# Kernel optimization log

Measured on AMD Instinct MI355X. Metric: run time of the kernel, lower is better.

## Reference

```python
import jax, jax.numpy as jnp
import numpy as np
from jax import lax

B, S, D, H = 128, 256, 64, 512
H2 = 2 * H          # decoder / bi-encoder hidden size
GE = 4 * H          # encoder LSTM gate size (per direction)
GD = 4 * H2         # decoder LSTM gate size
T = 60              # hard-coded decode length


def _w(k, shape):
    return jax.random.normal(k, shape, dtype=jnp.float32) * 0.05


def setup_inputs() -> dict:
    ks = iter(jax.random.split(jax.random.key(0), 32))
    inp = {"x": jax.random.normal(next(ks), (B, S, D), jnp.float32)}
    inp["enc0_Wih"] = _w(next(ks), (2, GE, D))
    inp["enc0_Whh"] = _w(next(ks), (2, GE, H))
    inp["enc0_b"] = _w(next(ks), (2, GE))
    inp["enc1_Wih"] = _w(next(ks), (2, GE, H2))
    inp["enc1_Whh"] = _w(next(ks), (2, GE, H))
    inp["enc1_b"] = _w(next(ks), (2, GE))
    for n in ("attn1", "attn2", "attn3"):
        inp[n + "_W"] = _w(next(ks), (H2, H2))
        inp[n + "_b"] = _w(next(ks), (H2,))
    inp["dec1_Wih"] = _w(next(ks), (GD, H2 + D))
    inp["dec1_Whh"] = _w(next(ks), (GD, H2))
    inp["dec1_b"] = _w(next(ks), (GD,))
    inp["dec2_Wih"] = _w(next(ks), (GD, 2 * H2))
    inp["dec2_Whh"] = _w(next(ks), (GD, H2))
    inp["dec2_b"] = _w(next(ks), (GD,))
    inp["dec3_Wih"] = _w(next(ks), (GD, 2 * H2))
    inp["dec3_Whh"] = _w(next(ks), (GD, H2))
    inp["dec3_b"] = _w(next(ks), (GD,))
    inp["out_W"] = _w(next(ks), (D, H2))
    inp["out_b"] = _w(next(ks), (D,))
    return inp


def _lstm_gates(g, c):
    i, f, gg, o = jnp.split(g, 4, axis=-1)  # torch gate order: i, f, g, o
    c = jax.nn.sigmoid(f) * c + jax.nn.sigmoid(i) * jnp.tanh(gg)
    h = jax.nn.sigmoid(o) * jnp.tanh(c)
    return h, c


def _lstm_layer(x, Wih, Whh, b, reverse):
    # x: [B,S,Din] -> hidden sequence [B,S,Hn]
    Bn = x.shape[0]
    Hn = Whh.shape[1]
    xg = jnp.einsum('bsd,gd->bsg', x, Wih) + b  # precompute input contributions

    def step(carry, xt):
        h, c = carry
        h, c = _lstm_gates(xt + h @ Whh.T, c)
        return (h, c), h

    init = (jnp.zeros((Bn, Hn), x.dtype), jnp.zeros((Bn, Hn), x.dtype))
    _, hs = lax.scan(step, init, jnp.swapaxes(xg, 0, 1), reverse=reverse)
    return jnp.swapaxes(hs, 0, 1)


def _bilstm(x, Wih, Whh, b):
    fwd = _lstm_layer(x, Wih[0], Whh[0], b[0], False)
    bwd = _lstm_layer(x, Wih[1], Whh[1], b[1], True)
    return jnp.concatenate([fwd, bwd], axis=-1)


def _cell(inp, h, c, Wih, Whh, b):
    return _lstm_gates(inp @ Wih.T + h @ Whh.T + b, c)


def _forward(x, enc0_Wih, enc0_Whh, enc0_b, enc1_Wih, enc1_Whh, enc1_b,
             attn1_W, attn1_b, attn2_W, attn2_b, attn3_W, attn3_b,
             dec1_Wih, dec1_Whh, dec1_b, dec2_Wih, dec2_Whh, dec2_b,
             dec3_Wih, dec3_Whh, dec3_b, out_W, out_b):
    Bn = x.shape[0]
    enc_out = _bilstm(_bilstm(x, enc0_Wih, enc0_Whh, enc0_b),
                      enc1_Wih, enc1_Whh, enc1_b)          # [B,S,2H]
    keys1 = enc_out @ attn1_W.T + attn1_b                  # [B,S,2H]
    keys2 = enc_out @ attn2_W.T + attn2_b
    keys3 = enc_out @ attn3_W.T + attn3_b

    def attend(h, keys):
        a = jax.nn.softmax(jnp.einsum('bd,bsd->bs', h, keys), axis=-1)
        return jnp.einsum('bs,bsd->bd', a, enc_out)        # [B,2H]

    z = jnp.zeros((Bn, H2), x.dtype)
    carry0 = (z, z, z, z, z, z, x[:, -1, :])

    def step(carry, _):
        h1, c1, h2, c2, h3, c3, prev = carry
        ctx1 = attend(h1, keys1)
        h1, c1 = _cell(jnp.concatenate([ctx1, prev], -1), h1, c1,
                       dec1_Wih, dec1_Whh, dec1_b)
        ctx2 = attend(h2, keys2)
        h2, c2 = _cell(jnp.concatenate([ctx2, h1], -1), h2, c2,
                       dec2_Wih, dec2_Whh, dec2_b)
        ctx3 = attend(h3, keys3)
        h3, c3 = _cell(jnp.concatenate([ctx3, h2], -1), h3, c3,
                       dec3_Wih, dec3_Whh, dec3_b)
        yt = h3 @ out_W.T + out_b                          # [B,D]
        return (h1, c1, h2, c2, h3, c3, yt), yt

    _, ys = lax.scan(step, carry0, None, length=T)         # [T,B,D]
    return jnp.swapaxes(ys, 0, 1)                          # [B,T,D]


def reference(x, enc0_Wih, enc0_Whh, enc0_b, enc1_Wih, enc1_Whh, enc1_b,
              attn1_W, attn1_b, attn2_W, attn2_b, attn3_W, attn3_b,
              dec1_Wih, dec1_Whh, dec1_b, dec2_Wih, dec2_Whh, dec2_b,
              dec3_Wih, dec3_Whh, dec3_b, out_W, out_b):
    return _forward(x, enc0_Wih, enc0_Whh, enc0_b, enc1_Wih, enc1_Whh, enc1_b,
                    attn1_W, attn1_b, attn2_W, attn2_b, attn3_W, attn3_b,
                    dec1_Wih, dec1_Whh, dec1_b, dec2_Wih, dec2_Whh, dec2_b,
                    dec3_Wih, dec3_Whh, dec3_b, out_W, out_b)
```

## Files before the change

### kernel.cpp

```cpp
#include <hip/hip_runtime.h>

typedef unsigned short u16;
typedef unsigned int u32;
typedef short v8s __attribute__((ext_vector_type(8)));
typedef float v4f __attribute__((ext_vector_type(4)));

#define DEV static __device__ __forceinline__

DEV float bf2f(u16 u) { union { u32 i; float f; } v; v.i = ((u32)u) << 16; return v.f; }
DEV u16 f2bf(float f) {
  union { float f; u32 i; } v; v.f = f;
  u32 i = v.i + 0x7FFFu + ((v.i >> 16) & 1u);
  return (u16)(i >> 16);
}
DEV float sigm(float x) { return 1.0f / (1.0f + __expf(-x)); }
DEV v4f mfma16(v8s a, v8s b, v4f c) {
  return __builtin_amdgcn_mfma_f32_16x16x32_bf16(a, b, c, 0, 0, 0);
}
DEV v8s ld8(const u16* p) { return *(const v8s*)p; }

DEV void gbar(u32* flags, int nwg, int wg, u32 tgt) {
  __syncthreads();
  if (threadIdx.x < 64) {
    if (threadIdx.x == 0) {
      __threadfence();
      __hip_atomic_store(flags + wg, tgt, __ATOMIC_RELEASE, __HIP_MEMORY_SCOPE_AGENT);
    }
    const int lane = threadIdx.x;
    for (;;) {
      bool ok = true;
      for (int i = lane; i < nwg; i += 64) {
        u32 v = __hip_atomic_load(flags + i, __ATOMIC_RELAXED, __HIP_MEMORY_SCOPE_AGENT);
        ok &= (v >= tgt);
      }
      if (__ballot((int)ok) == ~0ull) break;
      __builtin_amdgcn_s_sleep(1);
    }
    __threadfence();
  }
  __syncthreads();
}

__global__ void k_zero(uint4* p, int n) {
  int i = blockIdx.x * 256 + threadIdx.x;
  if (i < n) p[i] = make_uint4(0, 0, 0, 0);
}

__global__ void k_cvt(const float* __restrict__ s, u16* __restrict__ d, int n) {
  int i = (blockIdx.x * 256 + threadIdx.x) * 4;
  if (i < n) {
    float4 v = *(const float4*)(s + i);
    ushort4 u;
    u.x = f2bf(v.x); u.y = f2bf(v.y); u.z = f2bf(v.z); u.w = f2bf(v.w);
    *(ushort4*)(d + i) = u;
  }
}

__global__ void k_pack_enc(const float* __restrict__ Wih, const float* __restrict__ Whh,
                           const float* __restrict__ bsrc, u16* __restrict__ Wf,
                           float* __restrict__ bf, int DIN) {
  const int K = DIN + 512;
  const int bx = blockIdx.x;
  const int dir = bx >> 11, r = bx & 2047;
  const int g = (r >> 2) & 3, j = ((r >> 4) << 2) | (r & 3);
  const int orig = g * 512 + j;
  const float* wi = Wih + ((size_t)dir * 2048 + orig) * DIN;
  const float* wh = Whh + ((size_t)dir * 2048 + orig) * 512;
  u16* dst = Wf + ((size_t)dir * 2048 + r) * K;
  for (int k = threadIdx.x; k < K; k += 256)
    dst[k] = f2bf(k < DIN ? wi[k] : wh[k - DIN]);
  if (threadIdx.x == 0) bf[dir * 2048 + r] = bsrc[dir * 2048 + orig];
}

__global__ void k_pack_decf(const float* __restrict__ Wih, const float* __restrict__ Whh,
                            const float* __restrict__ bsrc, u16* __restrict__ Wf,
                            float* __restrict__ bf, int KIN) {
  const int K = KIN + 1024;
  const int r = blockIdx.x;
  const int g = (r >> 2) & 3, j = ((r >> 4) << 2) | (r & 3);
  const int orig = g * 1024 + j;
  const float* wi = Wih + (size_t)orig * KIN;
  const float* wh = Whh + (size_t)orig * 1024;
  const int wgi = r >> 4, l15 = r & 15;
  u16* dst = Wf + (size_t)wgi * (size_t)(K >> 5) * 512;
  for (int k = threadIdx.x; k < K; k += 256) {
    float v = k < KIN ? wi[k] : wh[k - KIN];
    dst[(size_t)(k >> 5) * 512 + (((k >> 3) & 3) * 16 + l15) * 8 + (k & 7)] = f2bf(v);
  }
  if (threadIdx.x == 0) bf[r] = bsrc[orig];
}

__global__ void k_pack_attnT(const float* __restrict__ w1, const float* __restrict__ w2,
                             const float* __restrict__ w3, u16* __restrict__ WQ) {
  const int a = blockIdx.x >> 10, tix = blockIdx.x & 1023;
  const int ti = tix >> 5, tj = tix & 31;
  const float* Wsrc = a == 0 ? w1 : (a == 1 ? w2 : w3);
  __shared__ float tl[32][33];
  const int r = threadIdx.x >> 3, c4 = (threadIdx.x & 7) * 4;
  const float* src = Wsrc + (size_t)(ti * 32 + r) * 1024 + tj * 32 + c4;
#pragma unroll
  for (int k = 0; k < 4; ++k) tl[r][c4 + k] = src[k];
  __syncthreads();
  const int cl = threadIdx.x >> 3, d4 = (threadIdx.x & 7) * 4;
  ushort4 u;
  u.x = f2bf(tl[d4 + 0][cl]); u.y = f2bf(tl[d4 + 1][cl]);
  u.z = f2bf(tl[d4 + 2][cl]); u.w = f2bf(tl[d4 + 3][cl]);
  *(ushort4*)(WQ + ((size_t)a << 20) + (size_t)(tj * 32 + cl) * 1024 + ti * 32 + d4) = u;
}

__global__ __launch_bounds__(512, 1) void k_rec(
    const u16* __restrict__ in, int DIN,
    const u16* __restrict__ Wf, const float* __restrict__ bias,
    u16* __restrict__ XG, u16* __restrict__ hst, u16* __restrict__ outp,
    u32* __restrict__ flags) {
  const int K = DIN + 512;
  const int DINk = DIN >> 5;
  const int wg = blockIdx.x;
  const int dir = wg >> 7, nt = wg & 127;
  const int r0 = nt * 16;
  const int tid = threadIdx.x, w = tid >> 6, lane = tid & 63;
  const int l15 = lane & 15, qd = lane >> 4;

  __shared__ u16 wlds[48 * 512];
  __shared__ float glds[128][17];

  {
    const u16* Wd = Wf + ((size_t)(dir * 2048 + r0)) * K;
    const int cnt = 16 * (K >> 3);
    for (int idx = tid; idx < cnt; idx += 512) {
      const int row = idx & 15, c8 = idx >> 4;
      uint4 v = *(const uint4*)(Wd + (size_t)row * K + c8 * 8);
      *(uint4*)(wlds + ((size_t)(c8 >> 2) * 512 + ((c8 & 3) * 16 + row) * 8)) = v;
    }
  }
  const int pm = tid >> 2, jl = tid & 3;
  float bw[4];
#pragma unroll
  for (int g = 0; g < 4; ++g) bw[g] = bias[dir * 2048 + r0 + g * 4 + jl];
  float cst = 0.f;
  __syncthreads();

  u32 bt = 1;
  if (DIN == 64) {
    for (int t = 0; t < 256; ++t) {
      const int tt = dir ? (255 - t) : t;
      const int pb = t & 1;
      const u16* xp = in + ((size_t)(w * 16 + l15) * 256 + tt) * 64 + qd * 8;
      const u16* hp = hst + ((size_t)((dir * 2 + pb) * 128 + w * 16 + l15)) * 512 + qd * 8;
      v4f a0 = mfma16(ld8(xp), ld8(wlds + lane * 8), (v4f){0.f, 0.f, 0.f, 0.f});
      v4f a1 = mfma16(ld8(xp + 32), ld8(wlds + 512 + lane * 8), (v4f){0.f, 0.f, 0.f, 0.f});
#pragma unroll 4
      for (int kkb = 0; kkb < 16; kkb += 2) {
        a0 = mfma16(ld8(hp + kkb * 32), ld8(wlds + (2 + kkb) * 512 + lane * 8), a0);
        a1 = mfma16(ld8(hp + kkb * 32 + 32), ld8(wlds + (3 + kkb) * 512 + lane * 8), a1);
      }
#pragma unroll
      for (int r = 0; r < 4; ++r)
        glds[w * 16 + qd * 4 + r][l15] = a0[r] + a1[r];
      __syncthreads();
      {
        float gi = glds[pm][0 * 4 + jl] + bw[0];
        float gf = glds[pm][1 * 4 + jl] + bw[1];
        float gg = glds[pm][2 * 4 + jl] + bw[2];
        float go = glds[pm][3 * 4 + jl] + bw[3];
        float cc = sigm(gf) * cst + sigm(gi) * tanhf(gg);
        cst = cc;
        u16 hb = f2bf(sigm(go) * tanhf(cc));
        hst[((size_t)((dir * 2 + (pb ^ 1)) * 128 + pm)) * 512 + nt * 4 + jl] = hb;
        outp[((size_t)pm * 256 + tt) * 1024 + dir * 512 + nt * 4 + jl] = hb;
      }
      gbar(flags + dir * 128, 128, nt, bt++);
    }
  } else {
    for (int ch = 0; ch < 32; ++ch) {
      for (int ttl = 0; ttl < 8; ++ttl) {
        const int tt = dir ? (255 - ch * 8 - ttl) : (ch * 8 + ttl);
        const u16* ap = in + ((size_t)(w * 16 + l15) * 256 + tt) * DIN + qd * 8;
        v4f a0 = (v4f){0.f, 0.f, 0.f, 0.f}, a1 = a0;
#pragma unroll 4
        for (int kkb = 0; kkb < 32; kkb += 2) {
          a0 = mfma16(ld8(ap + kkb * 32), ld8(wlds + kkb * 512 + lane * 8), a0);
          a1 = mfma16(ld8(ap + kkb * 32 + 32), ld8(wlds + (kkb + 1) * 512 + lane * 8), a1);
        }
        u16* xo = XG + (((size_t)(dir * 8 + ttl) * 128 + nt) * 128 + w * 16 + qd * 4) * 16 + l15;
#pragma unroll
        for (int r = 0; r < 4; ++r) xo[r * 16] = f2bf(a0[r] + a1[r]);
      }
      for (int ts = 0; ts < 8; ++ts) {
        const int t = ch * 8 + ts;
        const int tt = dir ? (255 - t) : t;
        const int pb = t & 1;
        const u16* hp = hst + ((size_t)((dir * 2 + pb) * 128 + w * 16 + l15)) * 512 + qd * 8;
        v4f a0 = (v4f){0.f, 0.f, 0.f, 0.f}, a1 = a0;
#pragma unroll 4
        for (int kkb = 0; kkb < 16; kkb += 2) {
          a0 = mfma16(ld8(hp + kkb * 32), ld8(wlds + (32 + kkb) * 512 + lane * 8), a0);
          a1 = mfma16(ld8(hp + kkb * 32 + 32), ld8(wlds + (33 + kkb) * 512 + lane * 8), a1);
        }
        const u16* xi = XG + (((size_t)(dir * 8 + ts) * 128 + nt) * 128 + w * 16 + qd * 4) * 16 + l15;
#pragma unroll
        for (int r = 0; r < 4; ++r)
          glds[w * 16 + qd * 4 + r][l15] = a0[r] + a1[r] + bf2f(xi[r * 16]);
        __syncthreads();
        {
          float gi = glds[pm][0 * 4 + jl] + bw[0];
          float gf = glds[pm][1 * 4 + jl] + bw[1];
          float gg = glds[pm][2 * 4 + jl] + bw[2];
          float go = glds[pm][3 * 4 + jl] + bw[3];
          float cc = sigm(gf) * cst + sigm(gi) * tanhf(gg);
          cst = cc;
          u16 hb = f2bf(sigm(go) * tanhf(cc));
          hst[((size_t)((dir * 2 + (pb ^ 1)) * 128 + pm)) * 512 + nt * 4 + jl] = hb;
          outp[((size_t)pm * 256 + tt) * 1024 + dir * 512 + nt * 4 + jl] = hb;
        }
        gbar(flags + dir * 128, 128, nt, bt++);
      }
    }
  }
}

struct DecArgs {
  const float *x, *outb;
  float* dout;
  const u16 *eo, *wq, *wout, *wd1, *wd2, *wd3;
  const float *bd1, *bd2, *bd3;
  u16 *qp, *hd, *ad1, *ad2, *ad3;
  u32* flags;
};

union DecSm {
  struct { float glds[128][17]; } c;
  struct {
    u16 e[32][1032];
    float sbuf[8][16][4];
    float wl[32][4];
    float alpha[4];
    float lfin[4];
  } a;
};

__global__ __launch_bounds__(512, 1) void k_dec(DecArgs A) {
  const int wg = blockIdx.x, tid = threadIdx.x;
  const int w = tid >> 6, lane = tid & 63, l15 = lane & 15, qd = lane >> 4;
  __shared__ DecSm sm;
  u32 bt = 1;

  const int cm_ = tid >> 2, cjl = tid & 3;
  const float* BDs[3] = {A.bd1, A.bd2, A.bd3};
  float cbias[3][4];
#pragma unroll
  for (int ci = 0; ci < 3; ++ci)
#pragma unroll
    for (int g = 0; g < 4; ++g)
      cbias[ci][g] = BDs[ci][wg * 16 + g * 4 + cjl];
  float cstate[3] = {0.f, 0.f, 0.f};

  for (int t = 0; t <= 60; ++t) {
    const int p = t & 1;
    if (wg < 192) {
      const int a = wg / 64, nc0 = (wg & 63) * 16;
      const u16* Ab = A.hd + (size_t)((a * 2 + p) * 128 + w * 16 + l15) * 1024 + qd * 8;
      const u16* Bw = A.wq + ((size_t)a << 20) + (size_t)(nc0 + l15) * 1024 + qd * 8;
      v4f a0 = (v4f){0.f, 0.f, 0.f, 0.f}, a1 = a0;
#pragma unroll 4
      for (int kk = 0; kk < 1024; kk += 64) {
        a0 = mfma16(ld8(Ab + kk), ld8(Bw + kk), a0);
        a1 = mfma16(ld8(Ab + kk + 32), ld8(Bw + kk + 32), a1);
      }
#pragma unroll
      for (int r = 0; r < 4; ++r)
        A.qp[(size_t)(w * 16 + qd * 4 + r) * 16384 + a * 1024 + nc0 + l15] =
            f2bf(a0[r] + a1[r]);
    } else if (wg < 196) {
      const int mt4 = wg - 192;
      if (t == 0) {
        int base = (mt4 * 512 + tid) * 4;
        int b = base >> 6, o = base & 63;
        const float* xs = A.x + (size_t)b * 16384 + 255 * 64 + o;
        u16* dst = A.ad1 + (size_t)b * 2112 + 1024 + o;
#pragma unroll
        for (int k2 = 0; k2 < 4; ++k2) dst[k2] = f2bf(xs[k2]);
      } else {
        const int mb = mt4 * 32 + (w >> 2) * 16, nb = (w & 3) * 16;
        const u16* Ab = A.hd + (size_t)((2 * 2 + p) * 128 + mb + l15) * 1024 + qd * 8;
        const u16* Bw = A.wout + (size_t)(nb + l15) * 1024 + qd * 8;
        v4f a0 = (v4f){0.f, 0.f, 0.f, 0.f}, a1 = a0;
#pragma unroll 4
        for (int kk = 0; kk < 1024; kk += 64) {
          a0 = mfma16(ld8(Ab + kk), ld8(Bw + kk), a0);
          a1 = mfma16(ld8(Ab + kk + 32), ld8(Bw + kk + 32), a1);
        }
        const int o = nb + l15;
        const float bo = A.outb[o];
#pragma unroll
        for (int r = 0; r < 4; ++r) {
          int m = mb + qd * 4 + r;
          float y = a0[r] + a1[r] + bo;
          A.dout[(size_t)m * 3840 + (t - 1) * 64 + o] = y;
          A.ad1[(size_t)m * 2112 + 1024 + o] = f2bf(y);
        }
      }
    }
    gbar(A.flags, 256, wg, bt++);
    if (t == 60) break;

    if (wg < 128) {
      const int b = wg;
      const u16* eob = A.eo + (size_t)b * 256 * 1024;
      v8s qf[8];
      {
        const u16* qsrc = A.qp + (size_t)b * 16384 + (size_t)l15 * 1024 + (w & 3) * 256 + qd * 8;
#pragma unroll
        for (int i = 0; i < 8; ++i) qf[i] = ld8(qsrc + i * 32);
      }
      const int d0 = w * 128 + lane * 2;
      float pv[3][2] = {{0.f, 0.f}, {0.f, 0.f}, {0.f, 0.f}};
      float mml0 = -3e38f, mml1 = -3e38f, mml2 = -3e38f;
      float lll0 = 0.f, lll1 = 0.f, lll2 = 0.f;
      const int sr = tid >> 4, sc = (tid & 15) * 8;
#pragma unroll
      for (int i = 0; i < 8; ++i)
        *(uint4*)&sm.a.e[sr][sc + i * 128] =
            *(const uint4*)(eob + (size_t)sr * 1024 + sc + i * 128);
      __syncthreads();

      for (int c = 0; c < 8; ++c) {
        uint4 pf[8];
        if (c < 7) {
          const u16* src = eob + (size_t)((c + 1) * 32 + sr) * 1024 + sc;
#pragma unroll
          for (int i = 0; i < 8; ++i) pf[i] = *(const uint4*)(src + i * 128);
        }
        {
          v4f sa = (v4f){0.f, 0.f, 0.f, 0.f};
          const u16* eb = &sm.a.e[(w >> 2) * 16 + l15][(w & 3) * 256 + qd * 8];
#pragma unroll
          for (int i = 0; i < 8; ++i) sa = mfma16(qf[i], ld8(eb + i * 32), sa);
          if (lane < 16) *(v4f*)&sm.a.sbuf[w][lane][0] = sa;
        }
        __syncthreads();
        if (tid < 32) {
          const int s = tid, sbb = s >> 4, sl = s & 15;
          float sc0 = 0.f, sc1 = 0.f, sc2 = 0.f;
#pragma unroll
          for (int k = 0; k < 4; ++k) {
            const float* sp = &sm.a.sbuf[sbb * 4 + k][sl][0];
            sc0 += sp[0]; sc1 += sp[1]; sc2 += sp[2];
          }
          float c0 = sc0, c1 = sc1, c2 = sc2;
#pragma unroll
          for (int m = 16; m >= 1; m >>= 1) {
            c0 = fmaxf(c0, __shfl_xor(c0, m));
            c1 = fmaxf(c1, __shfl_xor(c1, m));
            c2 = fmaxf(c2, __shfl_xor(c2, m));
          }
          float n0 = fmaxf(mml0, c0), n1 = fmaxf(mml1, c1), n2 = fmaxf(mml2, c2);
          float a0 = __expf(mml0 - n0), a1 = __expf(mml1 - n1), a2 = __expf(mml2 - n2);
          mml0 = n0; mml1 = n1; mml2 = n2;
          float w0 = __expf(sc0 - n0), w1 = __expf(sc1 - n1), w2 = __expf(sc2 - n2);
          sm.a.wl[s][0] = w0; sm.a.wl[s][1] = w1; sm.a.wl[s][2] = w2;
          float t0 = w0, t1 = w1, t2 = w2;
#pragma unroll
          for (int m = 16; m >= 1; m >>= 1) {
            t0 += __shfl_xor(t0, m); t1 += __shfl_xor(t1, m); t2 += __shfl_xor(t2, m);
          }
          lll0 = lll0 * a0 + t0; lll1 = lll1 * a1 + t1; lll2 = lll2 * a2 + t2;
          if (s == 0) {
            sm.a.alpha[0] = a0; sm.a.alpha[1] = a1; sm.a.alpha[2] = a2;
            sm.a.lfin[0] = lll0; sm.a.lfin[1] = lll1; sm.a.lfin[2] = lll2;
          }
        }
        __syncthreads();
        {
          const float a0 = sm.a.alpha[0], a1 = sm.a.alpha[1], a2 = sm.a.alpha[2];
          pv[0][0] *= a0; pv[0][1] *= a0;
          pv[1][0] *= a1; pv[1][1] *= a1;
          pv[2][0] *= a2; pv[2][1] *= a2;
#pragma unroll 4
          for (int s = 0; s < 32; ++s) {
            const float w0 = sm.a.wl[s][0], w1 = sm.a.wl[s][1], w2 = sm.a.wl[s][2];
            u32 ee = *(const u32*)&sm.a.e[s][d0];
            float e0 = bf2f((u16)ee), e1 = bf2f((u16)(ee >> 16));
            pv[0][0] += w0 * e0; pv[0][1] += w0 * e1;
            pv[1][0] += w1 * e0; pv[1][1] += w1 * e1;
            pv[2][0] += w2 * e0; pv[2][1] += w2 * e1;
          }
        }
        __syncthreads();
        if (c < 7) {
#pragma unroll
          for (int i = 0; i < 8; ++i)
            *(uint4*)&sm.a.e[sr][sc + i * 128] = pf[i];
        }
        __syncthreads();
      }
      {
        const float il0 = 1.0f / sm.a.lfin[0], il1 = 1.0f / sm.a.lfin[1],
                    il2 = 1.0f / sm.a.lfin[2];
        u32 p0 = (u32)f2bf(pv[0][0] * il0) | ((u32)f2bf(pv[0][1] * il0) << 16);
        u32 p1 = (u32)f2bf(pv[1][0] * il1) | ((u32)f2bf(pv[1][1] * il1) << 16);
        u32 p2 = (u32)f2bf(pv[2][0] * il2) | ((u32)f2bf(pv[2][1] * il2) << 16);
        *(u32*)&A.ad1[(size_t)b * 2112 + d0] = p0;
        *(u32*)&A.ad2[(size_t)b * 3072 + d0] = p1;
        *(u32*)&A.ad3[(size_t)b * 3072 + d0] = p2;
      }
    } else {
      const int b = wg - 128;
      const u16* h1 = A.hd + (size_t)((0 * 2 + p) * 128 + b) * 1024;
      const u16* h2 = A.hd + (size_t)((1 * 2 + p) * 128 + b) * 1024;
      const u16* h3 = A.hd + (size_t)((2 * 2 + p) * 128 + b) * 1024;
      if (tid < 128) {
        *(uint4*)(A.ad1 + (size_t)b * 2112 + 1088 + tid * 8) = *(const uint4*)(h1 + tid * 8);
      } else if (tid < 256) {
        int c8 = tid - 128;
        *(uint4*)(A.ad2 + (size_t)b * 3072 + 2048 + c8 * 8) = *(const uint4*)(h2 + c8 * 8);
      } else if (tid < 384) {
        int c8 = tid - 256;
        *(uint4*)(A.ad3 + (size_t)b * 3072 + 2048 + c8 * 8) = *(const uint4*)(h3 + c8 * 8);
      }
    }
    gbar(A.flags, 256, wg, bt++);

#pragma unroll
    for (int ci = 0; ci < 3; ++ci) {
      const int Kc = (ci == 0) ? 2112 : 3072;
      const u16* wb = (ci == 0 ? A.wd1 : ci == 1 ? A.wd2 : A.wd3) +
                      (size_t)wg * (size_t)(Kc >> 5) * 512;
      const u16* Ac = (ci == 0 ? A.ad1 : ci == 1 ? A.ad2 : A.ad3);
      {
        const u16* Ab = Ac + (size_t)(w * 16 + l15) * Kc + qd * 8;
        v4f a0 = (v4f){0.f, 0.f, 0.f, 0.f}, a1 = a0;
        const int NKB = Kc >> 5;
#pragma unroll 4
        for (int kkb = 0; kkb < NKB; kkb += 2) {
          a0 = mfma16(ld8(Ab + kkb * 32), ld8(wb + kkb * 512 + lane * 8), a0);
          a1 = mfma16(ld8(Ab + kkb * 32 + 32), ld8(wb + (kkb + 1) * 512 + lane * 8), a1);
        }
#pragma unroll
        for (int r = 0; r < 4; ++r)
          sm.c.glds[w * 16 + qd * 4 + r][l15] = a0[r] + a1[r];
      }
      __syncthreads();
      {
        float gi = sm.c.glds[cm_][0 * 4 + cjl] + cbias[ci][0];
        float gf = sm.c.glds[cm_][1 * 4 + cjl] + cbias[ci][1];
        float gg = sm.c.glds[cm_][2 * 4 + cjl] + cbias[ci][2];
        float go = sm.c.glds[cm_][3 * 4 + cjl] + cbias[ci][3];
        float cv = sigm(gf) * cstate[ci] + sigm(gi) * tanhf(gg);
        cstate[ci] = cv;
        u16 hb = f2bf(sigm(go) * tanhf(cv));
        const int jg = wg * 4 + cjl;
        A.hd[(size_t)((ci * 2 + (p ^ 1)) * 128 + cm_) * 1024 + jg] = hb;
        if (ci == 0) A.ad2[(size_t)cm_ * 3072 + 1024 + jg] = hb;
        else if (ci == 1) A.ad3[(size_t)cm_ * 3072 + 1024 + jg] = hb;
      }
      gbar(A.flags, 256, wg, bt++);
    }
  }
}

extern "C" void kernel_launch(void* const* d_in, const int* in_sizes, int n_in,
                              void* d_out, int out_size, void* d_ws, size_t ws_size,
                              hipStream_t stream) {
  char* ws = (char*)d_ws;
  size_t off = 0;
  auto alc = [&](size_t bytes) -> char* {
    char* pp = ws + off;
    off += (bytes + 255) & ~(size_t)255;
    return pp;
  };
  u16* XB = (u16*)alc(2097152ull * 2);
  u16* WF0 = (u16*)alc(2359296ull * 2);
  float* BF0 = (float*)alc(4096ull * 4);
  u16* WF1 = (u16*)alc(6291456ull * 2);
  float* BF1 = (float*)alc(4096ull * 4);
  u16* H0 = (u16*)alc(33554432ull * 2);
  u16* EO = (u16*)alc(33554432ull * 2);
  u16* HS0 = (u16*)alc(262144ull * 2);
  u16* HS1 = (u16*)alc(262144ull * 2);
  u16* XG = (u16*)alc(4194304ull * 2);
  u16* WQ = (u16*)alc(3145728ull * 2);
  u16* WOUT = (u16*)alc(65536ull * 2);
  u16* WD1 = (u16*)alc(8650752ull * 2);
  float* BD1 = (float*)alc(4096ull * 4);
  u16* WD2 = (u16*)alc(12582912ull * 2);
  float* BD2 = (float*)alc(4096ull * 4);
  u16* WD3 = (u16*)alc(12582912ull * 2);
  float* BD3 = (float*)alc(4096ull * 4);
  u16* QP = (u16*)alc(2097152ull * 2);
  u16* HD = (u16*)alc(786432ull * 2);
  u16* AD1 = (u16*)alc(270336ull * 2);
  u16* AD2 = (u16*)alc(393216ull * 2);
  u16* AD3 = (u16*)alc(393216ull * 2);
  u32* FLAGS = (u32*)alc(1536ull * 4);

  k_zero<<<2, 256, 0, stream>>>((uint4*)FLAGS, 384);
  k_zero<<<1024, 256, 0, stream>>>((uint4*)QP, 262144);
  k_zero<<<128, 256, 0, stream>>>((uint4*)HS0, 32768);
  k_zero<<<128, 256, 0, stream>>>((uint4*)HS1, 32768);
  k_zero<<<384, 256, 0, stream>>>((uint4*)HD, 98304);

  k_cvt<<<2048, 256, 0, stream>>>((const float*)d_in[0], XB, 2097152);
  k_cvt<<<64, 256, 0, stream>>>((const float*)d_in[22], WOUT, 65536);
  k_pack_enc<<<4096, 256, 0, stream>>>((const float*)d_in[1], (const float*)d_in[2],
                                       (const float*)d_in[3], WF0, BF0, 64);
  k_pack_enc<<<4096, 256, 0, stream>>>((const float*)d_in[4], (const float*)d_in[5],
                                       (const float*)d_in[6], WF1, BF1, 1024);
  k_pack_attnT<<<3072, 256, 0, stream>>>((const float*)d_in[7], (const float*)d_in[9],
                                         (const float*)d_in[11], WQ);
  k_pack_decf<<<4096, 256, 0, stream>>>((const float*)d_in[13], (const float*)d_in[14],
                                        (const float*)d_in[15], WD1, BD1, 1088);
  k_pack_decf<<<4096, 256, 0, stream>>>((const float*)d_in[16], (const float*)d_in[17],
                                        (const float*)d_in[18], WD2, BD2, 2048);
  k_pack_decf<<<4096, 256, 0, stream>>>((const float*)d_in[19], (const float*)d_in[20],
                                        (const float*)d_in[21], WD3, BD3, 2048);

  k_rec<<<256, 512, 0, stream>>>(XB, 64, WF0, BF0, XG, HS0, H0, FLAGS);
  k_rec<<<256, 512, 0, stream>>>(H0, 1024, WF1, BF1, XG, HS1, EO, FLAGS + 256);

  DecArgs da;
  da.x = (const float*)d_in[0];
  da.outb = (const float*)d_in[23];
  da.dout = (float*)d_out;
  da.eo = EO; da.wq = WQ; da.wout = WOUT;
  da.wd1 = WD1; da.wd2 = WD2; da.wd3 = WD3;
  da.bd1 = BD1; da.bd2 = BD2; da.bd3 = BD3;
  da.qp = QP; da.hd = HD; da.ad1 = AD1; da.ad2 = AD2; da.ad3 = AD3;
  da.flags = FLAGS + 512;
  k_dec<<<256, 512, 0, stream>>>(da);
}
```

Baseline: 29.97 ms.

## Replace grid-barrier fences with relaxed atomic data accesses and pack LSTM cell stores

Drops the __threadfence calls around the grid barrier and the release ordering on the flag store. In their place, all cross-workgroup data exchanged between barriers (hidden states, attention outputs, query projections, decoder inputs) is read and written through agent-scope relaxed atomic loads and stores. The LSTM cell update now has each thread compute two adjacent hidden units and write packed 32-bit values. Query and output-projection results are staged through LDS so they go out as wider stores. The aim is to cut per-step fence and barrier latency in the sequential recurrent loops, but memory-ordering correctness now depends on relaxed atomics without explicit fences.

```diff
diff --git a/kernel.cpp b/kernel.cpp
--- a/kernel.cpp
+++ b/kernel.cpp
@@ -2,6 +2,7 @@
 
 typedef unsigned short u16;
 typedef unsigned int u32;
+typedef unsigned long long u64;
 typedef short v8s __attribute__((ext_vector_type(8)));
 typedef float v4f __attribute__((ext_vector_type(4)));
 
@@ -19,13 +20,27 @@
 }
 DEV v8s ld8(const u16* p) { return *(const v8s*)p; }
 
+DEV u64 ldg64(const u16* p) {
+  return __hip_atomic_load((const u64*)p, __ATOMIC_RELAXED, __HIP_MEMORY_SCOPE_AGENT);
+}
+DEV void stg32(u16* p, u32 v) {
+  __hip_atomic_store((u32*)p, v, __ATOMIC_RELAXED, __HIP_MEMORY_SCOPE_AGENT);
+}
+DEV void stg64(u16* p, u64 v) {
+  __hip_atomic_store((u64*)p, v, __ATOMIC_RELAXED, __HIP_MEMORY_SCOPE_AGENT);
+}
+DEV v8s ld8c(const u16* p) {
+  union { u64 q[2]; v8s v; } u;
+  u.q[0] = ldg64(p);
+  u.q[1] = ldg64(p + 4);
+  return u.v;
+}
+
 DEV void gbar(u32* flags, int nwg, int wg, u32 tgt) {
   __syncthreads();
+  if (threadIdx.x == 0)
+    __hip_atomic_store(flags + wg, tgt, __ATOMIC_RELAXED, __HIP_MEMORY_SCOPE_AGENT);
   if (threadIdx.x < 64) {
-    if (threadIdx.x == 0) {
-      __threadfence();
-      __hip_atomic_store(flags + wg, tgt, __ATOMIC_RELEASE, __HIP_MEMORY_SCOPE_AGENT);
-    }
     const int lane = threadIdx.x;
     for (;;) {
       bool ok = true;
@@ -36,7 +51,6 @@
       if (__ballot((int)ok) == ~0ull) break;
       __builtin_amdgcn_s_sleep(1);
     }
-    __threadfence();
   }
   __syncthreads();
 }
@@ -114,7 +128,6 @@
     u16* __restrict__ XG, u16* __restrict__ hst, u16* __restrict__ outp,
     u32* __restrict__ flags) {
   const int K = DIN + 512;
-  const int DINk = DIN >> 5;
   const int wg = blockIdx.x;
   const int dir = wg >> 7, nt = wg & 127;
   const int r0 = nt * 16;
@@ -133,11 +146,14 @@
       *(uint4*)(wlds + ((size_t)(c8 >> 2) * 512 + ((c8 & 3) * 16 + row) * 8)) = v;
     }
   }
-  const int pm = tid >> 2, jl = tid & 3;
-  float bw[4];
-#pragma unroll
-  for (int g = 0; g < 4; ++g) bw[g] = bias[dir * 2048 + r0 + g * 4 + jl];
-  float cst = 0.f;
+  const int pm = tid >> 1, jp = tid & 1;
+  float bw[4][2];
+#pragma unroll
+  for (int g = 0; g < 4; ++g)
+#pragma unroll
+    for (int jj = 0; jj < 2; ++jj)
+      bw[g][jj] = bias[dir * 2048 + r0 + g * 4 + jp * 2 + jj];
+  float cst[2] = {0.f, 0.f};
   __syncthreads();
 
   u32 bt = 1;
@@ -151,23 +167,29 @@
       v4f a1 = mfma16(ld8(xp + 32), ld8(wlds + 512 + lane * 8), (v4f){0.f, 0.f, 0.f, 0.f});
 #pragma unroll 4
       for (int kkb = 0; kkb < 16; kkb += 2) {
-        a0 = mfma16(ld8(hp + kkb * 32), ld8(wlds + (2 + kkb) * 512 + lane * 8), a0);
-        a1 = mfma16(ld8(hp + kkb * 32 + 32), ld8(wlds + (3 + kkb) * 512 + lane * 8), a1);
+        a0 = mfma16(ld8c(hp + kkb * 32), ld8(wlds + (2 + kkb) * 512 + lane * 8), a0);
+        a1 = mfma16(ld8c(hp + kkb * 32 + 32), ld8(wlds + (3 + kkb) * 512 + lane * 8), a1);
       }
 #pragma unroll
       for (int r = 0; r < 4; ++r)
         glds[w * 16 + qd * 4 + r][l15] = a0[r] + a1[r];
       __syncthreads();
-      {
-        float gi = glds[pm][0 * 4 + jl] + bw[0];
-        float gf = glds[pm][1 * 4 + jl] + bw[1];
-        float gg = glds[pm][2 * 4 + jl] + bw[2];
-        float go = glds[pm][3 * 4 + jl] + bw[3];
-        float cc = sigm(gf) * cst + sigm(gi) * tanhf(gg);
-        cst = cc;
-        u16 hb = f2bf(sigm(go) * tanhf(cc));
-        hst[((size_t)((dir * 2 + (pb ^ 1)) * 128 + pm)) * 512 + nt * 4 + jl] = hb;
-        outp[((size_t)pm * 256 + tt) * 1024 + dir * 512 + nt * 4 + jl] = hb;
+      if (tid < 256) {
+        float hv2[2];
+#pragma unroll
+        for (int jj = 0; jj < 2; ++jj) {
+          const int jl = jp * 2 + jj;
+          float gi = glds[pm][0 * 4 + jl] + bw[0][jj];
+          float gf = glds[pm][1 * 4 + jl] + bw[1][jj];
+          float gg = glds[pm][2 * 4 + jl] + bw[2][jj];
+          float go = glds[pm][3 * 4 + jl] + bw[3][jj];
+          float cc = sigm(gf) * cst[jj] + sigm(gi) * tanhf(gg);
+          cst[jj] = cc;
+          hv2[jj] = sigm(go) * tanhf(cc);
+        }
+        u32 hv = (u32)f2bf(hv2[0]) | ((u32)f2bf(hv2[1]) << 16);
+        stg32(hst + ((size_t)((dir * 2 + (pb ^ 1)) * 128 + pm)) * 512 + nt * 4 + jp * 2, hv);
+        *(u32*)(outp + ((size_t)pm * 256 + tt) * 1024 + dir * 512 + nt * 4 + jp * 2) = hv;
       }
       gbar(flags + dir * 128, 128, nt, bt++);
     }
@@ -175,7 +197,7 @@
     for (int ch = 0; ch < 32; ++ch) {
       for (int ttl = 0; ttl < 8; ++ttl) {
         const int tt = dir ? (255 - ch * 8 - ttl) : (ch * 8 + ttl);
-        const u16* ap = in + ((size_t)(w * 16 + l15) * 256 + tt) * DIN + qd * 8;
+        const u16* ap = in + ((size_t)(w * 16 + l15) * 256 + tt) * 1024 + qd * 8;
         v4f a0 = (v4f){0.f, 0.f, 0.f, 0.f}, a1 = a0;
 #pragma unroll 4
         for (int kkb = 0; kkb < 32; kkb += 2) {
@@ -194,24 +216,30 @@
         v4f a0 = (v4f){0.f, 0.f, 0.f, 0.f}, a1 = a0;
 #pragma unroll 4
         for (int kkb = 0; kkb < 16; kkb += 2) {
-          a0 = mfma16(ld8(hp + kkb * 32), ld8(wlds + (32 + kkb) * 512 + lane * 8), a0);
-          a1 = mfma16(ld8(hp + kkb * 32 + 32), ld8(wlds + (33 + kkb) * 512 + lane * 8), a1);
+          a0 = mfma16(ld8c(hp + kkb * 32), ld8(wlds + (32 + kkb) * 512 + lane * 8), a0);
+          a1 = mfma16(ld8c(hp + kkb * 32 + 32), ld8(wlds + (33 + kkb) * 512 + lane * 8), a1);
         }
         const u16* xi = XG + (((size_t)(dir * 8 + ts) * 128 + nt) * 128 + w * 16 + qd * 4) * 16 + l15;
 #pragma unroll
         for (int r = 0; r < 4; ++r)
           glds[w * 16 + qd * 4 + r][l15] = a0[r] + a1[r] + bf2f(xi[r * 16]);
         __syncthreads();
-        {
-          float gi = glds[pm][0 * 4 + jl] + bw[0];
-          float gf = glds[pm][1 * 4 + jl] + bw[1];
-          float gg = glds[pm][2 * 4 + jl] + bw[2];
-          float go = glds[pm][3 * 4 + jl] + bw[3];
-          float cc = sigm(gf) * cst + sigm(gi) * tanhf(gg);
-          cst = cc;
-          u16 hb = f2bf(sigm(go) * tanhf(cc));
-          hst[((size_t)((dir * 2 + (pb ^ 1)) * 128 + pm)) * 512 + nt * 4 + jl] = hb;
-          outp[((size_t)pm * 256 + tt) * 1024 + dir * 512 + nt * 4 + jl] = hb;
+        if (tid < 256) {
+          float hv2[2];
+#pragma unroll
+          for (int jj = 0; jj < 2; ++jj) {
+            const int jl = jp * 2 + jj;
+            float gi = glds[pm][0 * 4 + jl] + bw[0][jj];
+            float gf = glds[pm][1 * 4 + jl] + bw[1][jj];
+            float gg = glds[pm][2 * 4 + jl] + bw[2][jj];
+            float go = glds[pm][3 * 4 + jl] + bw[3][jj];
+            float cc = sigm(gf) * cst[jj] + sigm(gi) * tanhf(gg);
+            cst[jj] = cc;
+            hv2[jj] = sigm(go) * tanhf(cc);
+          }
+          u32 hv = (u32)f2bf(hv2[0]) | ((u32)f2bf(hv2[1]) << 16);
+          stg32(hst + ((size_t)((dir * 2 + (pb ^ 1)) * 128 + pm)) * 512 + nt * 4 + jp * 2, hv);
+          *(u32*)(outp + ((size_t)pm * 256 + tt) * 1024 + dir * 512 + nt * 4 + jp * 2) = hv;
         }
         gbar(flags + dir * 128, 128, nt, bt++);
       }
@@ -230,6 +258,7 @@
 
 union DecSm {
   struct { float glds[128][17]; } c;
+  struct { float yb[32][65]; } y;
   struct {
     u16 e[32][1032];
     float sbuf[8][16][4];
@@ -245,15 +274,17 @@
   __shared__ DecSm sm;
   u32 bt = 1;
 
-  const int cm_ = tid >> 2, cjl = tid & 3;
+  const int cm_ = tid >> 1, cjp = tid & 1;
   const float* BDs[3] = {A.bd1, A.bd2, A.bd3};
-  float cbias[3][4];
+  float cbias[3][4][2];
 #pragma unroll
   for (int ci = 0; ci < 3; ++ci)
 #pragma unroll
     for (int g = 0; g < 4; ++g)
-      cbias[ci][g] = BDs[ci][wg * 16 + g * 4 + cjl];
-  float cstate[3] = {0.f, 0.f, 0.f};
+#pragma unroll
+      for (int jj = 0; jj < 2; ++jj)
+        cbias[ci][g][jj] = BDs[ci][wg * 16 + g * 4 + cjp * 2 + jj];
+  float cstate[3][2] = {{0.f, 0.f}, {0.f, 0.f}, {0.f, 0.f}};
 
   for (int t = 0; t <= 60; ++t) {
     const int p = t & 1;
@@ -264,13 +295,22 @@
       v4f a0 = (v4f){0.f, 0.f, 0.f, 0.f}, a1 = a0;
 #pragma unroll 4
       for (int kk = 0; kk < 1024; kk += 64) {
-        a0 = mfma16(ld8(Ab + kk), ld8(Bw + kk), a0);
-        a1 = mfma16(ld8(Ab + kk + 32), ld8(Bw + kk + 32), a1);
+        a0 = mfma16(ld8c(Ab + kk), ld8(Bw + kk), a0);
+        a1 = mfma16(ld8c(Ab + kk + 32), ld8(Bw + kk + 32), a1);
       }
 #pragma unroll
       for (int r = 0; r < 4; ++r)
-        A.qp[(size_t)(w * 16 + qd * 4 + r) * 16384 + a * 1024 + nc0 + l15] =
-            f2bf(a0[r] + a1[r]);
+        sm.c.glds[w * 16 + qd * 4 + r][l15] = a0[r] + a1[r];
+      __syncthreads();
+      {
+        const int m = tid >> 2, c4 = (tid & 3) * 4;
+        const float* row = &sm.c.glds[m][0];
+        u32 lo = (u32)f2bf(row[c4]) | ((u32)f2bf(row[c4 + 1]) << 16);
+        u32 hi = (u32)f2bf(row[c4 + 2]) | ((u32)f2bf(row[c4 + 3]) << 16);
+        u16* qdst = A.qp + (size_t)m * 16384 + a * 1024 + nc0 + c4;
+        stg32(qdst, lo);
+        stg32(qdst + 2, hi);
+      }
     } else if (wg < 196) {
       const int mt4 = wg - 192;
       if (t == 0) {
@@ -278,8 +318,8 @@
         int b = base >> 6, o = base & 63;
         const float* xs = A.x + (size_t)b * 16384 + 255 * 64 + o;
         u16* dst = A.ad1 + (size_t)b * 2112 + 1024 + o;
-#pragma unroll
-        for (int k2 = 0; k2 < 4; ++k2) dst[k2] = f2bf(xs[k2]);
+        stg32(dst, (u32)f2bf(xs[0]) | ((u32)f2bf(xs[1]) << 16));
+        stg32(dst + 2, (u32)f2bf(xs[2]) | ((u32)f2bf(xs[3]) << 16));
       } else {
         const int mb = mt4 * 32 + (w >> 2) * 16, nb = (w & 3) * 16;
         const u16* Ab = A.hd + (size_t)((2 * 2 + p) * 128 + mb + l15) * 1024 + qd * 8;
@@ -287,17 +327,24 @@
         v4f a0 = (v4f){0.f, 0.f, 0.f, 0.f}, a1 = a0;
 #pragma unroll 4
         for (int kk = 0; kk < 1024; kk += 64) {
-          a0 = mfma16(ld8(Ab + kk), ld8(Bw + kk), a0);
-          a1 = mfma16(ld8(Ab + kk + 32), ld8(Bw + kk + 32), a1);
-        }
-        const int o = nb + l15;
-        const float bo = A.outb[o];
-#pragma unroll
-        for (int r = 0; r < 4; ++r) {
-          int m = mb + qd * 4 + r;
-          float y = a0[r] + a1[r] + bo;
-          A.dout[(size_t)m * 3840 + (t - 1) * 64 + o] = y;
-          A.ad1[(size_t)m * 2112 + 1024 + o] = f2bf(y);
+          a0 = mfma16(ld8c(Ab + kk), ld8(Bw + kk), a0);
+          a1 = mfma16(ld8c(Ab + kk + 32), ld8(Bw + kk + 32), a1);
+        }
+        const int mloc = (w >> 2) * 16 + qd * 4;
+#pragma unroll
+        for (int r = 0; r < 4; ++r)
+          sm.y.yb[mloc + r][nb + l15] = a0[r] + a1[r] + A.outb[nb + l15];
+        __syncthreads();
+        {
+          const int ml = tid >> 4, c4 = (tid & 15) * 4;
+          const int mg = mt4 * 32 + ml;
+          float y0 = sm.y.yb[ml][c4], y1 = sm.y.yb[ml][c4 + 1];
+          float y2 = sm.y.yb[ml][c4 + 2], y3 = sm.y.yb[ml][c4 + 3];
+          float4 yv = {y0, y1, y2, y3};
+          *(float4*)(A.dout + (size_t)mg * 3840 + (t - 1) * 64 + c4) = yv;
+          u16* dst = A.ad1 + (size_t)mg * 2112 + 1024 + c4;
+          stg32(dst, (u32)f2bf(y0) | ((u32)f2bf(y1) << 16));
+          stg32(dst + 2, (u32)f2bf(y2) | ((u32)f2bf(y3) << 16));
         }
       }
     }
@@ -311,7 +358,7 @@
       {
         const u16* qsrc = A.qp + (size_t)b * 16384 + (size_t)l15 * 1024 + (w & 3) * 256 + qd * 8;
 #pragma unroll
-        for (int i = 0; i < 8; ++i) qf[i] = ld8(qsrc + i * 32);
+        for (int i = 0; i < 8; ++i) qf[i] = ld8c(qsrc + i * 32);
       }
       const int d0 = w * 128 + lane * 2;
       float pv[3][2] = {{0.f, 0.f}, {0.f, 0.f}, {0.f, 0.f}};
@@ -397,27 +444,26 @@
       {
         const float il0 = 1.0f / sm.a.lfin[0], il1 = 1.0f / sm.a.lfin[1],
                     il2 = 1.0f / sm.a.lfin[2];
-        u32 p0 = (u32)f2bf(pv[0][0] * il0) | ((u32)f2bf(pv[0][1] * il0) << 16);
-        u32 p1 = (u32)f2bf(pv[1][0] * il1) | ((u32)f2bf(pv[1][1] * il1) << 16);
-        u32 p2 = (u32)f2bf(pv[2][0] * il2) | ((u32)f2bf(pv[2][1] * il2) << 16);
-        *(u32*)&A.ad1[(size_t)b * 2112 + d0] = p0;
-        *(u32*)&A.ad2[(size_t)b * 3072 + d0] = p1;
-        *(u32*)&A.ad3[(size_t)b * 3072 + d0] = p2;
+        stg32(A.ad1 + (size_t)b * 2112 + d0,
+              (u32)f2bf(pv[0][0] * il0) | ((u32)f2bf(pv[0][1] * il0) << 16));
+        stg32(A.ad2 + (size_t)b * 3072 + d0,
+              (u32)f2bf(pv[1][0] * il1) | ((u32)f2bf(pv[1][1] * il1) << 16));
+        stg32(A.ad3 + (size_t)b * 3072 + d0,
+              (u32)f2bf(pv[2][0] * il2) | ((u32)f2bf(pv[2][1] * il2) << 16));
       }
     } else {
       const int b = wg - 128;
       const u16* h1 = A.hd + (size_t)((0 * 2 + p) * 128 + b) * 1024;
       const u16* h2 = A.hd + (size_t)((1 * 2 + p) * 128 + b) * 1024;
       const u16* h3 = A.hd + (size_t)((2 * 2 + p) * 128 + b) * 1024;
-      if (tid < 128) {
-        *(uint4*)(A.ad1 + (size_t)b * 2112 + 1088 + tid * 8) = *(const uint4*)(h1 + tid * 8);
-      } else if (tid < 256) {
-        int c8 = tid - 128;
-        *(uint4*)(A.ad2 + (size_t)b * 3072 + 2048 + c8 * 8) = *(const uint4*)(h2 + c8 * 8);
-      } else if (tid < 384) {
-        int c8 = tid - 256;
-        *(uint4*)(A.ad3 + (size_t)b * 3072 + 2048 + c8 * 8) = *(const uint4*)(h3 + c8 * 8);
-      }
+      if (tid < 256) {
+        stg64(A.ad1 + (size_t)b * 2112 + 1088 + tid * 4, ldg64(h1 + tid * 4));
+      } else if (tid < 512) {
+        int c4 = tid - 256;
+        stg64(A.ad2 + (size_t)b * 3072 + 2048 + c4 * 4, ldg64(h2 + c4 * 4));
+      }
+      if (tid < 256)
+        stg64(A.ad3 + (size_t)b * 3072 + 2048 + tid * 4, ldg64(h3 + tid * 4));
     }
     gbar(A.flags, 256, wg, bt++);
 
@@ -433,26 +479,32 @@
         const int NKB = Kc >> 5;
 #pragma unroll 4
         for (int kkb = 0; kkb < NKB; kkb += 2) {
-          a0 = mfma16(ld8(Ab + kkb * 32), ld8(wb + kkb * 512 + lane * 8), a0);
-          a1 = mfma16(ld8(Ab + kkb * 32 + 32), ld8(wb + (kkb + 1) * 512 + lane * 8), a1);
+          a0 = mfma16(ld8c(Ab + kkb * 32), ld8(wb + kkb * 512 + lane * 8), a0);
+          a1 = mfma16(ld8c(Ab + kkb * 32 + 32), ld8(wb + (kkb + 1) * 512 + lane * 8), a1);
         }
 #pragma unroll
         for (int r = 0; r < 4; ++r)
           sm.c.glds[w * 16 + qd * 4 + r][l15] = a0[r] + a1[r];
       }
       __syncthreads();
-      {
-        float gi = sm.c.glds[cm_][0 * 4 + cjl] + cbias[ci][0];
-        float gf = sm.c.glds[cm_][1 * 4 + cjl] + cbias[ci][1];
-        float gg = sm.c.glds[cm_][2 * 4 + cjl] + cbias[ci][2];
-        float go = sm.c.glds[cm_][3 * 4 + cjl] + cbias[ci][3];
-        float cv = sigm(gf) * cstate[ci] + sigm(gi) * tanhf(gg);
-        cstate[ci] = cv;
-        u16 hb = f2bf(sigm(go) * tanhf(cv));
-        const int jg = wg * 4 + cjl;
-        A.hd[(size_t)((ci * 2 + (p ^ 1)) * 128 + cm_) * 1024 + jg] = hb;
-        if (ci == 0) A.ad2[(size_t)cm_ * 3072 + 1024 + jg] = hb;
-        else if (ci == 1) A.ad3[(size_t)cm_ * 3072 + 1024 + jg] = hb;
+      if (tid < 256) {
+        float hv2[2];
+#pragma unroll
+        for (int jj = 0; jj < 2; ++jj) {
+          const int jl = cjp * 2 + jj;
+          float gi = sm.c.glds[cm_][0 * 4 + jl] + cbias[ci][0][jj];
+          float gf = sm.c.glds[cm_][1 * 4 + jl] + cbias[ci][1][jj];
+          float gg = sm.c.glds[cm_][2 * 4 + jl] + cbias[ci][2][jj];
+          float go = sm.c.glds[cm_][3 * 4 + jl] + cbias[ci][3][jj];
+          float cv = sigm(gf) * cstate[ci][jj] + sigm(gi) * tanhf(gg);
+          cstate[ci][jj] = cv;
+          hv2[jj] = sigm(go) * tanhf(cv);
+        }
+        u32 hv = (u32)f2bf(hv2[0]) | ((u32)f2bf(hv2[1]) << 16);
+        const int jg = wg * 4 + cjp * 2;
+        stg32(A.hd + (size_t)((ci * 2 + (p ^ 1)) * 128 + cm_) * 1024 + jg, hv);
+        if (ci == 0) stg32(A.ad2 + (size_t)cm_ * 3072 + 1024 + jg, hv);
+        else if (ci == 1) stg32(A.ad3 + (size_t)cm_ * 3072 + 1024 + jg, hv);
       }
       gbar(A.flags, 256, wg, bt++);
     }
```

New measurement: 25.05 ms. 16.4% less time.
